# Performance work log

Measured on AMD Instinct MI355X. Metric: run time of the kernel, lower is better.

## Reference

```python
import jax, jax.numpy as jnp
import numpy as np

N, E = 30000, 480000
IN_C, HID, HEADS = 128, 32, 8
HC = HID * HEADS  # 256
EPS = 1e-5
NEG_SLOPE = 0.2


def setup_inputs() -> dict:
    key = jax.random.key(0)
    ks = jax.random.split(key, 20)
    s = 0.05
    return {
        "x": jax.random.normal(ks[0], (N, IN_C), jnp.float32),
        "edge_index": jax.random.randint(ks[1], (2, E), 0, N, jnp.int32),
        "W1": jax.random.normal(ks[2], (IN_C, HC), jnp.float32) * s,
        "a1_src": jax.random.normal(ks[3], (HEADS, HID), jnp.float32) * s,
        "a1_dst": jax.random.normal(ks[4], (HEADS, HID), jnp.float32) * s,
        "b1": jnp.zeros((HC,), jnp.float32),
        "g1": jnp.ones((HC,), jnp.float32),
        "be1": jnp.zeros((HC,), jnp.float32),
        "W2": jax.random.normal(ks[5], (HC, HC), jnp.float32) * s,
        "a2_src": jax.random.normal(ks[6], (HEADS, HID), jnp.float32) * s,
        "a2_dst": jax.random.normal(ks[7], (HEADS, HID), jnp.float32) * s,
        "b2": jnp.zeros((HC,), jnp.float32),
        "g2": jnp.ones((HC,), jnp.float32),
        "be2": jnp.zeros((HC,), jnp.float32),
        "lW1": jax.random.normal(ks[8], (HC, HID), jnp.float32) * s,
        "lb1": jnp.zeros((HID,), jnp.float32),
        "lW2": jax.random.normal(ks[9], (HID, 1), jnp.float32) * s,
        "lb2": jnp.zeros((1,), jnp.float32),
    }


def gat_layer(x, src, dst, W, a_s, a_d, b):
    # x: [N, Fin] -> h: [N, H, C]
    h = (x @ W).reshape(N, HEADS, HID)
    al_s = jnp.sum(h * a_s, axis=-1)  # [N, H]
    al_d = jnp.sum(h * a_d, axis=-1)  # [N, H]
    e = jax.nn.leaky_relu(al_s[src] + al_d[dst], NEG_SLOPE)  # [E', H]
    # segment softmax over incoming edges of each destination node
    e = e - jax.ops.segment_max(e, dst, num_segments=N)[dst]
    ex = jnp.exp(e)
    alpha = ex / jax.ops.segment_sum(ex, dst, num_segments=N)[dst]
    msg = h[src] * alpha[:, :, None]  # [E', H, C]
    out = jax.ops.segment_sum(msg, dst, num_segments=N)  # [N, H, C]
    return out.reshape(N, HC) + b


def batchnorm(x, g, b):
    m = jnp.mean(x, axis=0)
    v = jnp.var(x, axis=0)
    return (x - m) * jax.lax.rsqrt(v + EPS) * g + b


def reference(x, edge_index, W1, a1_src, a1_dst, b1, g1, be1,
              W2, a2_src, a2_dst, b2, g2, be2, lW1, lb1, lW2, lb2):
    # add self-loops (PyG GATConv default)
    loop = jnp.arange(N, dtype=edge_index.dtype)
    src = jnp.concatenate([edge_index[0], loop])
    dst = jnp.concatenate([edge_index[1], loop])

    h = jax.nn.elu(gat_layer(x, src, dst, W1, a1_src, a1_dst, b1))
    h = batchnorm(h, g1, be1)
    h = jax.nn.elu(gat_layer(h, src, dst, W2, a2_src, a2_dst, b2))
    h = batchnorm(h, g2, be2)
    h = jax.nn.elu(h @ lW1 + lb1)
    return h @ lW2 + lb2
```

## Files before the change

kernel.cpp:

```cpp
#include <hip/hip_runtime.h>
#include <math.h>

#define N_NODES 30000
#define E_EDGES 480000
#define EP (E_EDGES + N_NODES)
#define IN_CH 128
#define HID 32
#define HEADS 8
#define HC 256
#define BN_EPS 1e-5f
#define NEG_SLOPE 0.2f
#define SCAN_NB ((N_NODES + 1023) / 1024)
#define PART_SLOTS 64

typedef __attribute__((ext_vector_type(8))) short bf16x8;
typedef __attribute__((ext_vector_type(4))) float f32x4;

__device__ __forceinline__ float elu_f(float x) { return x > 0.f ? x : __expf(x) - 1.f; }
__device__ __forceinline__ float lrelu_f(float x) { return x >= 0.f ? x : NEG_SLOPE * x; }
__device__ __forceinline__ float bf2f(unsigned short u) {
    return __uint_as_float(((unsigned)u) << 16);
}
__device__ __forceinline__ unsigned short f2bf(float f) {
    unsigned u = __float_as_uint(f);
    return (unsigned short)((u + 0x7fffu + ((u >> 16) & 1u)) >> 16);
}

__global__ void wt_all_kernel(const float* __restrict__ W1, const float* __restrict__ W2,
                              const float* __restrict__ lW1,
                              unsigned short* __restrict__ wt1,
                              unsigned short* __restrict__ wt2,
                              unsigned short* __restrict__ wtm) {
    int i = blockIdx.x * 256 + threadIdx.x;
    if (i < IN_CH * HC) {
        int k = i >> 8, n = i & 255;
        wt1[(size_t)n * IN_CH + k] = f2bf(W1[i]);
    } else if (i < IN_CH * HC + HC * HC) {
        int j = i - IN_CH * HC;
        int k = j >> 8, n = j & 255;
        wt2[(size_t)n * HC + k] = f2bf(W2[j]);
    } else if (i < IN_CH * HC + HC * HC + HC * HID) {
        int j = i - IN_CH * HC - HC * HC;
        int k = j >> 5, n = j & 31;
        wtm[(size_t)n * HC + k] = f2bf(lW1[j]);
    }
}

__global__ __launch_bounds__(256) void gemm_mfma(const float* __restrict__ A32,
                                                 const unsigned short* __restrict__ Abf,
                                                 const unsigned short* __restrict__ Bt,
                                                 unsigned short* __restrict__ C,
                                                 float* __restrict__ al_s,
                                                 float* __restrict__ al_d,
                                                 const float* __restrict__ a_src,
                                                 const float* __restrict__ a_dst,
                                                 int M, int K,
                                                 const float* __restrict__ sc,
                                                 const float* __restrict__ sh) {
    __shared__ __align__(16) unsigned short As[64][40];
    __shared__ __align__(16) unsigned short Bs[256][40];
    int tid = threadIdx.x;
    int wave = tid >> 6, lane = tid & 63;
    int m = lane & 15, q = lane >> 4;
    int row0 = blockIdx.x * 64;
    f32x4 acc[16];
#pragma unroll
    for (int i = 0; i < 16; ++i) acc[i] = (f32x4){0.f, 0.f, 0.f, 0.f};
    int ar = tid >> 2, aseg = tid & 3;
    for (int k0 = 0; k0 < K; k0 += 32) {
        float4 v0 = make_float4(0.f, 0.f, 0.f, 0.f), v1 = v0;
        int gr = row0 + ar;
        int c0 = k0 + aseg * 8;
        if (gr < M) {
            if (A32) {
                const float* ap = A32 + (size_t)gr * K + c0;
                v0 = *(const float4*)ap;
                v1 = *(const float4*)(ap + 4);
            } else {
                uint4 raw = *(const uint4*)(Abf + (size_t)gr * K + c0);
                v0.x = bf2f((unsigned short)raw.x); v0.y = bf2f((unsigned short)(raw.x >> 16));
                v0.z = bf2f((unsigned short)raw.y); v0.w = bf2f((unsigned short)(raw.y >> 16));
                v1.x = bf2f((unsigned short)raw.z); v1.y = bf2f((unsigned short)(raw.z >> 16));
                v1.z = bf2f((unsigned short)raw.w); v1.w = bf2f((unsigned short)(raw.w >> 16));
            }
        }
        if (sc) {
            float4 s0 = *(const float4*)(sc + c0), s1 = *(const float4*)(sc + c0 + 4);
            float4 t0 = *(const float4*)(sh + c0), t1 = *(const float4*)(sh + c0 + 4);
            v0.x = v0.x * s0.x + t0.x; v0.y = v0.y * s0.y + t0.y;
            v0.z = v0.z * s0.z + t0.z; v0.w = v0.w * s0.w + t0.w;
            v1.x = v1.x * s1.x + t1.x; v1.y = v1.y * s1.y + t1.y;
            v1.z = v1.z * s1.z + t1.z; v1.w = v1.w * s1.w + t1.w;
        }
        bf16x8 av;
        av[0] = (short)f2bf(v0.x); av[1] = (short)f2bf(v0.y);
        av[2] = (short)f2bf(v0.z); av[3] = (short)f2bf(v0.w);
        av[4] = (short)f2bf(v1.x); av[5] = (short)f2bf(v1.y);
        av[6] = (short)f2bf(v1.z); av[7] = (short)f2bf(v1.w);
        *(bf16x8*)(&As[ar][aseg * 8]) = av;
        const unsigned short* bp = Bt + (size_t)tid * K + k0;
#pragma unroll
        for (int sg = 0; sg < 4; ++sg)
            *(uint4*)(&Bs[tid][sg * 8]) = *(const uint4*)(bp + sg * 8);
        __syncthreads();
        bf16x8 a = *(const bf16x8*)(&As[wave * 16 + m][q * 8]);
#pragma unroll
        for (int nt = 0; nt < 16; ++nt) {
            bf16x8 b = *(const bf16x8*)(&Bs[nt * 16 + m][q * 8]);
            acc[nt] = __builtin_amdgcn_mfma_f32_16x16x32_bf16(a, b, acc[nt], 0, 0, 0);
        }
        __syncthreads();
    }
    int rbase = row0 + wave * 16;
    float asv[16], adv[16];
#pragma unroll
    for (int nt = 0; nt < 16; ++nt) {
        asv[nt] = a_src[nt * 16 + m];
        adv[nt] = a_dst[nt * 16 + m];
    }
#pragma unroll
    for (int r = 0; r < 4; ++r) {
        int grow = rbase + q * 4 + r;
        bool gv = grow < M;
        if (gv) {
#pragma unroll
            for (int nt = 0; nt < 16; ++nt)
                C[(size_t)grow * HC + nt * 16 + m] = f2bf(acc[nt][r]);
        }
#pragma unroll
        for (int h = 0; h < HEADS; ++h) {
            float ps = acc[2 * h][r] * asv[2 * h] + acc[2 * h + 1][r] * asv[2 * h + 1];
            float pd = acc[2 * h][r] * adv[2 * h] + acc[2 * h + 1][r] * adv[2 * h + 1];
            ps += __shfl_xor(ps, 1); pd += __shfl_xor(pd, 1);
            ps += __shfl_xor(ps, 2); pd += __shfl_xor(pd, 2);
            ps += __shfl_xor(ps, 4); pd += __shfl_xor(pd, 4);
            ps += __shfl_xor(ps, 8); pd += __shfl_xor(pd, 8);
            if (m == h && gv) {
                al_s[grow * HEADS + h] = ps;
                al_d[grow * HEADS + h] = pd;
            }
        }
    }
}

__global__ void deg_kernel(const int* __restrict__ ei, int* __restrict__ deg,
                           float* __restrict__ part) {
    int e = blockIdx.x * blockDim.x + threadIdx.x;
    if (e < 2 * PART_SLOTS * 512) part[e] = 0.f;
    if (e >= EP) return;
    int d = (e < E_EDGES) ? ei[E_EDGES + e] : e - E_EDGES;
    atomicAdd(deg + d, 1);
}

__global__ __launch_bounds__(1024) void scan_blk(const int* __restrict__ deg,
                                                 int* __restrict__ rs,
                                                 int* __restrict__ bsum) {
    __shared__ int sh[1024];
    int t = threadIdx.x;
    int i = blockIdx.x * 1024 + t;
    int v = (i < N_NODES) ? deg[i] : 0;
    sh[t] = v;
    __syncthreads();
    for (int off = 1; off < 1024; off <<= 1) {
        int tv = (t >= off) ? sh[t - off] : 0;
        __syncthreads();
        sh[t] += tv;
        __syncthreads();
    }
    if (i < N_NODES) rs[i] = sh[t] - v;
    if (t == 1023) bsum[blockIdx.x] = sh[1023];
}

__global__ __launch_bounds__(1024) void scan_add(int* __restrict__ rs,
                                                 int* __restrict__ cursor,
                                                 const int* __restrict__ bsum) {
    __shared__ int sh_off, sh_tot;
    int t = threadIdx.x;
    if (t < 64) {
        int v = (t < SCAN_NB) ? bsum[t] : 0;
        int pre = (t < (int)blockIdx.x) ? v : 0;
        int tot = v;
#pragma unroll
        for (int off = 1; off < 64; off <<= 1) {
            tot += __shfl_xor(tot, off);
            pre += __shfl_xor(pre, off);
        }
        if (t == 0) { sh_off = pre; sh_tot = tot; }
    }
    __syncthreads();
    int i = blockIdx.x * 1024 + t;
    if (i < N_NODES) {
        int v = rs[i] + sh_off;
        rs[i] = v;
        cursor[i] = v;
    } else if (i == N_NODES) {
        rs[N_NODES] = sh_tot;
    }
}

__global__ void scatter_kernel(const int* __restrict__ ei, int* __restrict__ cursor,
                               int* __restrict__ csr_src) {
    int e = blockIdx.x * blockDim.x + threadIdx.x;
    if (e >= EP) return;
    int s, d;
    if (e < E_EDGES) { s = ei[e]; d = ei[E_EDGES + e]; } else { s = d = e - E_EDGES; }
    int pos = atomicAdd(cursor + d, 1);
    csr_src[pos] = s;
}

__global__ __launch_bounds__(256) void attn_kernel(const uint4* __restrict__ h8,
                                                   const float* __restrict__ al_s,
                                                   const float* __restrict__ al_d,
                                                   const int* __restrict__ row_start,
                                                   const int* __restrict__ csr_src,
                                                   const float4* __restrict__ bias4,
                                                   uint4* __restrict__ out8,
                                                   float* __restrict__ part) {
    __shared__ float lds_s[4][256];
    __shared__ float lds_q[4][256];
    int wave = threadIdx.x >> 6;
    int d = blockIdx.x * 4 + wave;
    int lane = threadIdx.x & 63;
    int hh = lane & 7, eo = lane >> 3;
    int g = lane >> 5, c = lane & 31;
    int hl = c >> 2;
    int beg = row_start[d], end = row_start[d + 1];
    float ad = al_d[d * HEADS + hh];
    float ssum = 0.f;
    float acc[8];
#pragma unroll
    for (int t = 0; t < 8; ++t) acc[t] = 0.f;

#define PAIR_BODY(p)                                                      \
    {                                                                     \
        int e0 = 2 * (p) + g;                                             \
        int sj = __shfl(sreg, e0 * 8);                                    \
        float aj = __shfl(ex, e0 * 8 + hl);                               \
        uint4 v = h8[(size_t)sj * 32 + c];                                \
        acc[0] += aj * bf2f((unsigned short)v.x);                         \
        acc[1] += aj * bf2f((unsigned short)(v.x >> 16));                 \
        acc[2] += aj * bf2f((unsigned short)v.y);                         \
        acc[3] += aj * bf2f((unsigned short)(v.y >> 16));                 \
        acc[4] += aj * bf2f((unsigned short)v.z);                         \
        acc[5] += aj * bf2f((unsigned short)(v.z >> 16));                 \
        acc[6] += aj * bf2f((unsigned short)v.w);                         \
        acc[7] += aj * bf2f((unsigned short)(v.w >> 16));                 \
    }

    for (int i = beg; i < end; i += 8) {
        int chunk = end - i;
        if (chunk > 8) chunk = 8;
        int sreg = 0;
        float ex = 0.f;
        if (eo < chunk) {
            sreg = csr_src[i + eo];
            ex = __expf(lrelu_f(al_s[sreg * HEADS + hh] + ad));
        }
        ssum += ex;
        if (chunk == 8) {
#pragma unroll
            for (int p = 0; p < 4; ++p) PAIR_BODY(p);
        } else {
            int np = (chunk + 1) >> 1;
            for (int p = 0; p < np; ++p) PAIR_BODY(p);
        }
    }
#undef PAIR_BODY

#pragma unroll
    for (int t = 0; t < 8; ++t) acc[t] += __shfl_xor(acc[t], 32);
    ssum += __shfl_xor(ssum, 8);
    ssum += __shfl_xor(ssum, 16);
    ssum += __shfl_xor(ssum, 32);
    float inv = 1.f / __shfl(ssum, hl);

    float4 b0 = bias4[c * 2], b1 = bias4[c * 2 + 1];
    float o0 = elu_f(acc[0] * inv + b0.x);
    float o1 = elu_f(acc[1] * inv + b0.y);
    float o2 = elu_f(acc[2] * inv + b0.z);
    float o3 = elu_f(acc[3] * inv + b0.w);
    float o4 = elu_f(acc[4] * inv + b1.x);
    float o5 = elu_f(acc[5] * inv + b1.y);
    float o6 = elu_f(acc[6] * inv + b1.z);
    float o7 = elu_f(acc[7] * inv + b1.w);

    if (g == 0) {
        uint4 ov;
        ov.x = (unsigned)f2bf(o0) | ((unsigned)f2bf(o1) << 16);
        ov.y = (unsigned)f2bf(o2) | ((unsigned)f2bf(o3) << 16);
        ov.z = (unsigned)f2bf(o4) | ((unsigned)f2bf(o5) << 16);
        ov.w = (unsigned)f2bf(o6) | ((unsigned)f2bf(o7) << 16);
        out8[(size_t)d * 32 + c] = ov;
        int cb = c * 8;
        lds_s[wave][cb + 0] = o0; lds_q[wave][cb + 0] = o0 * o0;
        lds_s[wave][cb + 1] = o1; lds_q[wave][cb + 1] = o1 * o1;
        lds_s[wave][cb + 2] = o2; lds_q[wave][cb + 2] = o2 * o2;
        lds_s[wave][cb + 3] = o3; lds_q[wave][cb + 3] = o3 * o3;
        lds_s[wave][cb + 4] = o4; lds_q[wave][cb + 4] = o4 * o4;
        lds_s[wave][cb + 5] = o5; lds_q[wave][cb + 5] = o5 * o5;
        lds_s[wave][cb + 6] = o6; lds_q[wave][cb + 6] = o6 * o6;
        lds_s[wave][cb + 7] = o7; lds_q[wave][cb + 7] = o7 * o7;
    }
    __syncthreads();
    int ch = threadIdx.x;
    float s = lds_s[0][ch] + lds_s[1][ch] + lds_s[2][ch] + lds_s[3][ch];
    float q = lds_q[0][ch] + lds_q[1][ch] + lds_q[2][ch] + lds_q[3][ch];
    float* pb = part + (size_t)(blockIdx.x & (PART_SLOTS - 1)) * 512;
    atomicAdd(pb + ch, s);
    atomicAdd(pb + 256 + ch, q);
}

__global__ void bn_fin_kernel(const float* __restrict__ part,
                              const float* __restrict__ g, const float* __restrict__ be,
                              float* __restrict__ scale, float* __restrict__ shift) {
    int c = threadIdx.x;
    float s = 0.f, q = 0.f;
#pragma unroll
    for (int b = 0; b < PART_SLOTS; ++b) {
        s += part[(size_t)b * 512 + c];
        q += part[(size_t)b * 512 + 256 + c];
    }
    float m = s / (float)N_NODES;
    float var = q / (float)N_NODES - m * m;
    float istd = rsqrtf(var + BN_EPS);
    float sc = istd * g[c];
    scale[c] = sc;
    shift[c] = be[c] - m * sc;
}

__global__ __launch_bounds__(256) void mlp_mfma(const unsigned short* __restrict__ in,
                                                const float* __restrict__ sc,
                                                const float* __restrict__ sh,
                                                const unsigned short* __restrict__ Wt,
                                                const float* __restrict__ lb1,
                                                const float* __restrict__ lW2,
                                                const float* __restrict__ lb2,
                                                float* __restrict__ out) {
    int tid = threadIdx.x;
    int wave = tid >> 6, lane = tid & 63;
    int m = lane & 15, q = lane >> 4;
    int rbase = blockIdx.x * 64 + wave * 16;
    int arow = rbase + m;
    bool valid = arow < N_NODES;
    const unsigned short* ap = in + (size_t)arow * HC;
    f32x4 acc0 = (f32x4){0.f, 0.f, 0.f, 0.f}, acc1 = acc0;
#pragma unroll
    for (int k0 = 0; k0 < HC; k0 += 32) {
        int c0 = k0 + q * 8;
        bf16x8 b0 = *(const bf16x8*)(Wt + (size_t)m * HC + c0);
        bf16x8 b1 = *(const bf16x8*)(Wt + (size_t)(m + 16) * HC + c0);
        bf16x8 a = (bf16x8){0, 0, 0, 0, 0, 0, 0, 0};
        if (valid) {
            uint4 raw = *(const uint4*)(ap + c0);
            float v0 = bf2f((unsigned short)raw.x), v1 = bf2f((unsigned short)(raw.x >> 16));
            float v2 = bf2f((unsigned short)raw.y), v3 = bf2f((unsigned short)(raw.y >> 16));
            float v4 = bf2f((unsigned short)raw.z), v5 = bf2f((unsigned short)(raw.z >> 16));
            float v6 = bf2f((unsigned short)raw.w), v7 = bf2f((unsigned short)(raw.w >> 16));
            float4 s0 = *(const float4*)(sc + c0), s1 = *(const float4*)(sc + c0 + 4);
            float4 t0 = *(const float4*)(sh + c0), t1 = *(const float4*)(sh + c0 + 4);
            a[0] = (short)f2bf(v0 * s0.x + t0.x);
            a[1] = (short)f2bf(v1 * s0.y + t0.y);
            a[2] = (short)f2bf(v2 * s0.z + t0.z);
            a[3] = (short)f2bf(v3 * s0.w + t0.w);
            a[4] = (short)f2bf(v4 * s1.x + t1.x);
            a[5] = (short)f2bf(v5 * s1.y + t1.y);
            a[6] = (short)f2bf(v6 * s1.z + t1.z);
            a[7] = (short)f2bf(v7 * s1.w + t1.w);
        }
        acc0 = __builtin_amdgcn_mfma_f32_16x16x32_bf16(a, b0, acc0, 0, 0, 0);
        acc1 = __builtin_amdgcn_mfma_f32_16x16x32_bf16(a, b1, acc1, 0, 0, 0);
    }
    float w2a = lW2[m], w2b = lW2[m + 16];
    float ba = lb1[m], bb = lb1[m + 16];
#pragma unroll
    for (int r = 0; r < 4; ++r) {
        float v = elu_f(acc0[r] + ba) * w2a + elu_f(acc1[r] + bb) * w2b;
        v += __shfl_xor(v, 1);
        v += __shfl_xor(v, 2);
        v += __shfl_xor(v, 4);
        v += __shfl_xor(v, 8);
        int orow = rbase + q * 4 + r;
        if (m == 0 && orow < N_NODES) out[orow] = v + lb2[0];
    }
}

extern "C" void kernel_launch(void* const* d_in, const int* in_sizes, int n_in,
                              void* d_out, int out_size, void* d_ws, size_t ws_size,
                              hipStream_t stream) {
    const float* x   = (const float*)d_in[0];
    const int*   ei  = (const int*)d_in[1];
    const float* W1  = (const float*)d_in[2];
    const float* a1s = (const float*)d_in[3];
    const float* a1d = (const float*)d_in[4];
    const float* b1  = (const float*)d_in[5];
    const float* g1  = (const float*)d_in[6];
    const float* be1 = (const float*)d_in[7];
    const float* W2  = (const float*)d_in[8];
    const float* a2s = (const float*)d_in[9];
    const float* a2d = (const float*)d_in[10];
    const float* b2  = (const float*)d_in[11];
    const float* g2  = (const float*)d_in[12];
    const float* be2 = (const float*)d_in[13];
    const float* lW1 = (const float*)d_in[14];
    const float* lb1 = (const float*)d_in[15];
    const float* lW2 = (const float*)d_in[16];
    const float* lb2 = (const float*)d_in[17];
    float* out = (float*)d_out;

    char* p = (char*)d_ws;
    auto alloc = [&](size_t bytes) {
        char* r = p;
        p += (bytes + 255) & ~(size_t)255;
        return r;
    };
    unsigned short* h_bf  = (unsigned short*)alloc((size_t)N_NODES * HC * 2);
    unsigned short* o_bf  = (unsigned short*)alloc((size_t)N_NODES * HC * 2);
    unsigned short* wt1   = (unsigned short*)alloc((size_t)IN_CH * HC * 2);
    unsigned short* wt2   = (unsigned short*)alloc((size_t)HC * HC * 2);
    unsigned short* wtm   = (unsigned short*)alloc((size_t)HC * HID * 2);
    float* f_als  = (float*)alloc((size_t)N_NODES * HEADS * 4);
    float* f_ald  = (float*)alloc((size_t)N_NODES * HEADS * 4);
    int*   i_deg  = (int*)alloc((size_t)N_NODES * 4);
    int*   i_rs   = (int*)alloc((size_t)(N_NODES + 1) * 4);
    int*   i_cur  = (int*)alloc((size_t)N_NODES * 4);
    int*   i_src  = (int*)alloc((size_t)EP * 4);
    int*   i_bsum = (int*)alloc((size_t)(SCAN_NB + 1) * 4);
    float* f_part = (float*)alloc((size_t)2 * PART_SLOTS * 512 * 4);
    float* f_sc1  = (float*)alloc(HC * 4);
    float* f_sh1  = (float*)alloc(HC * 4);
    float* f_sc2  = (float*)alloc(HC * 4);
    float* f_sh2  = (float*)alloc(HC * 4);

    int eb = (EP + 255) / 256;

    hipMemsetAsync(i_deg, 0, (size_t)N_NODES * 4, stream);
    deg_kernel<<<eb, 256, 0, stream>>>(ei, i_deg, f_part);
    scan_blk<<<SCAN_NB, 1024, 0, stream>>>(i_deg, i_rs, i_bsum);
    scan_add<<<SCAN_NB, 1024, 0, stream>>>(i_rs, i_cur, i_bsum);
    scatter_kernel<<<eb, 256, 0, stream>>>(ei, i_cur, i_src);

    int wtot = IN_CH * HC + HC * HC + HC * HID;
    wt_all_kernel<<<(wtot + 255) / 256, 256, 0, stream>>>(W1, W2, lW1, wt1, wt2, wtm);

    int gblocks = (N_NODES + 63) / 64;

    auto run_layer = [&](const float* A32, const unsigned short* Abf, int K,
                         const unsigned short* wt, const float* in_sc, const float* in_sh,
                         const float* as_, const float* ad_, const float* bias,
                         const float* gam, const float* bet, float* part,
                         float* out_sc, float* out_sh) {
        gemm_mfma<<<gblocks, 256, 0, stream>>>(A32, Abf, wt, h_bf, f_als, f_ald, as_, ad_,
                                               N_NODES, K, in_sc, in_sh);
        attn_kernel<<<N_NODES / 4, 256, 0, stream>>>((const uint4*)h_bf, f_als, f_ald,
                                                     i_rs, i_src, (const float4*)bias,
                                                     (uint4*)o_bf, part);
        bn_fin_kernel<<<1, 256, 0, stream>>>(part, gam, bet, out_sc, out_sh);
    };

    run_layer(x, nullptr, IN_CH, wt1, nullptr, nullptr, a1s, a1d, b1, g1, be1,
              f_part, f_sc1, f_sh1);
    run_layer(nullptr, o_bf, HC, wt2, f_sc1, f_sh1, a2s, a2d, b2, g2, be2,
              f_part + (size_t)PART_SLOTS * 512, f_sc2, f_sh2);

    mlp_mfma<<<gblocks, 256, 0, stream>>>(o_bf, f_sc2, f_sh2, wtm, lb1, lW2, lb2, out);
}
```

Before: 302.8 us.

## Split attention aggregation across head-pair quarters via second grid dimension

The attention/aggregation kernel now launches a 2D grid in which each block handles one quarter of the channels (two heads) for four destination nodes. Each wave then processes eight edges at once, one per lane group, each lane loading a 16-byte slice of the source row for its head pair. Partial sums are reduced across edge groups with xor shuffles. This raises parallelism and memory-level concurrency per destination, at the cost of re-reading CSR indices and attention logits four times and doing extra shuffle reductions.

```diff
diff --git a/kernel.cpp b/kernel.cpp
--- a/kernel.cpp
+++ b/kernel.cpp
@@ -216,65 +216,59 @@
                                                    const float4* __restrict__ bias4,
                                                    uint4* __restrict__ out8,
                                                    float* __restrict__ part) {
-    __shared__ float lds_s[4][256];
-    __shared__ float lds_q[4][256];
+    __shared__ float lds_s[4][64];
+    __shared__ float lds_q[4][64];
     int wave = threadIdx.x >> 6;
     int d = blockIdx.x * 4 + wave;
+    int p = blockIdx.y;
     int lane = threadIdx.x & 63;
-    int hh = lane & 7, eo = lane >> 3;
-    int g = lane >> 5, c = lane & 31;
-    int hl = c >> 2;
+    int eo = lane >> 3, c = lane & 7;
     int beg = row_start[d], end = row_start[d + 1];
-    float ad = al_d[d * HEADS + hh];
+    float ad = al_d[d * HEADS + 2 * p + (c & 1)];
     float ssum = 0.f;
     float acc[8];
 #pragma unroll
     for (int t = 0; t < 8; ++t) acc[t] = 0.f;
 
-#define PAIR_BODY(p)                                                      \
-    {                                                                     \
-        int e0 = 2 * (p) + g;                                             \
-        int sj = __shfl(sreg, e0 * 8);                                    \
-        float aj = __shfl(ex, e0 * 8 + hl);                               \
-        uint4 v = h8[(size_t)sj * 32 + c];                                \
-        acc[0] += aj * bf2f((unsigned short)v.x);                         \
-        acc[1] += aj * bf2f((unsigned short)(v.x >> 16));                 \
-        acc[2] += aj * bf2f((unsigned short)v.y);                         \
-        acc[3] += aj * bf2f((unsigned short)(v.y >> 16));                 \
-        acc[4] += aj * bf2f((unsigned short)v.z);                         \
-        acc[5] += aj * bf2f((unsigned short)(v.z >> 16));                 \
-        acc[6] += aj * bf2f((unsigned short)v.w);                         \
-        acc[7] += aj * bf2f((unsigned short)(v.w >> 16));                 \
-    }
+    const uint4* hq = h8 + (size_t)p * 8;
 
     for (int i = beg; i < end; i += 8) {
-        int chunk = end - i;
-        if (chunk > 8) chunk = 8;
-        int sreg = 0;
+        int cnt = end - i;
+        if (cnt > 8) cnt = 8;
+        int sidx = i + (lane & 7);
+        if (sidx >= end) sidx = end - 1;
+        int sv = csr_src[sidx];
+        int sreg = __shfl(sv, eo);
         float ex = 0.f;
-        if (eo < chunk) {
-            sreg = csr_src[i + eo];
-            ex = __expf(lrelu_f(al_s[sreg * HEADS + hh] + ad));
-        }
+        if (c < 2 && eo < cnt)
+            ex = __expf(lrelu_f(al_s[sreg * HEADS + 2 * p + c] + ad));
         ssum += ex;
-        if (chunk == 8) {
-#pragma unroll
-            for (int p = 0; p < 4; ++p) PAIR_BODY(p);
-        } else {
-            int np = (chunk + 1) >> 1;
-            for (int p = 0; p < np; ++p) PAIR_BODY(p);
-        }
-    }
-#undef PAIR_BODY
-
-#pragma unroll
-    for (int t = 0; t < 8; ++t) acc[t] += __shfl_xor(acc[t], 32);
+        float aj = __shfl(ex, (lane & 56) + (c >> 2));
+        if (eo < cnt) {
+            uint4 v = hq[(size_t)sreg * 32 + c];
+            acc[0] += aj * bf2f((unsigned short)v.x);
+            acc[1] += aj * bf2f((unsigned short)(v.x >> 16));
+            acc[2] += aj * bf2f((unsigned short)v.y);
+            acc[3] += aj * bf2f((unsigned short)(v.y >> 16));
+            acc[4] += aj * bf2f((unsigned short)v.z);
+            acc[5] += aj * bf2f((unsigned short)(v.z >> 16));
+            acc[6] += aj * bf2f((unsigned short)v.w);
+            acc[7] += aj * bf2f((unsigned short)(v.w >> 16));
+        }
+    }
+
     ssum += __shfl_xor(ssum, 8);
     ssum += __shfl_xor(ssum, 16);
     ssum += __shfl_xor(ssum, 32);
-    float inv = 1.f / __shfl(ssum, hl);
-
-    float4 b0 = bias4[c * 2], b1 = bias4[c * 2 + 1];
+#pragma unroll
+    for (int t = 0; t < 8; ++t) {
+        acc[t] += __shfl_xor(acc[t], 8);
+        acc[t] += __shfl_xor(acc[t], 16);
+        acc[t] += __shfl_xor(acc[t], 32);
+    }
+    float inv = 1.f / __shfl(ssum, c >> 2);
+
+    float4 b0 = bias4[p * 16 + c * 2], b1 = bias4[p * 16 + c * 2 + 1];
     float o0 = elu_f(acc[0] * inv + b0.x);
     float o1 = elu_f(acc[1] * inv + b0.y);
     float o2 = elu_f(acc[2] * inv + b0.z);
@@ -284,13 +278,13 @@
     float o6 = elu_f(acc[6] * inv + b1.z);
     float o7 = elu_f(acc[7] * inv + b1.w);
 
-    if (g == 0) {
+    if (eo == 0) {
         uint4 ov;
         ov.x = (unsigned)f2bf(o0) | ((unsigned)f2bf(o1) << 16);
         ov.y = (unsigned)f2bf(o2) | ((unsigned)f2bf(o3) << 16);
         ov.z = (unsigned)f2bf(o4) | ((unsigned)f2bf(o5) << 16);
         ov.w = (unsigned)f2bf(o6) | ((unsigned)f2bf(o7) << 16);
-        out8[(size_t)d * 32 + c] = ov;
+        out8[(size_t)d * 32 + p * 8 + c] = ov;
         int cb = c * 8;
         lds_s[wave][cb + 0] = o0; lds_q[wave][cb + 0] = o0 * o0;
         lds_s[wave][cb + 1] = o1; lds_q[wave][cb + 1] = o1 * o1;
@@ -303,11 +297,13 @@
     }
     __syncthreads();
     int ch = threadIdx.x;
-    float s = lds_s[0][ch] + lds_s[1][ch] + lds_s[2][ch] + lds_s[3][ch];
-    float q = lds_q[0][ch] + lds_q[1][ch] + lds_q[2][ch] + lds_q[3][ch];
-    float* pb = part + (size_t)(blockIdx.x & (PART_SLOTS - 1)) * 512;
-    atomicAdd(pb + ch, s);
-    atomicAdd(pb + 256 + ch, q);
+    if (ch < 64) {
+        float s = lds_s[0][ch] + lds_s[1][ch] + lds_s[2][ch] + lds_s[3][ch];
+        float q = lds_q[0][ch] + lds_q[1][ch] + lds_q[2][ch] + lds_q[3][ch];
+        float* pb = part + (size_t)(blockIdx.x & (PART_SLOTS - 1)) * 512;
+        atomicAdd(pb + p * 64 + ch, s);
+        atomicAdd(pb + 256 + p * 64 + ch, q);
+    }
 }
 
 __global__ void bn_fin_kernel(const float* __restrict__ part,
@@ -451,9 +447,10 @@
                          float* out_sc, float* out_sh) {
         gemm_mfma<<<gblocks, 256, 0, stream>>>(A32, Abf, wt, h_bf, f_als, f_ald, as_, ad_,
                                                N_NODES, K, in_sc, in_sh);
-        attn_kernel<<<N_NODES / 4, 256, 0, stream>>>((const uint4*)h_bf, f_als, f_ald,
-                                                     i_rs, i_src, (const float4*)bias,
-                                                     (uint4*)o_bf, part);
+        dim3 agrid(N_NODES / 4, 4);
+        attn_kernel<<<agrid, 256, 0, stream>>>((const uint4*)h_bf, f_als, f_ald,
+                                               i_rs, i_src, (const float4*)bias,
+                                               (uint4*)o_bf, part);
         bn_fin_kernel<<<1, 256, 0, stream>>>(part, gam, bet, out_sc, out_sh);
     };
 
```

Measured after the change: 380.6 us. +25.7%, slower.
